# Optimization experiments

Hardware: AMD Instinct MI355X
Metric: run time of the kernel (lower is better)

## Reference

```python
import jax, jax.numpy as jnp
import numpy as np

EMB_DIM = 2048
USER_DIM = 256
NUM_EXPERTS = 64
TOP_K = 8
N_TOKENS = 16384


def setup_inputs() -> dict:
    key = jax.random.key(0)
    k_h, k_u, k_w = jax.random.split(key, 3)
    h = jax.random.normal(k_h, (N_TOKENS, EMB_DIM), dtype=jnp.float32)
    u = jax.random.normal(k_u, (N_TOKENS, USER_DIM), dtype=jnp.float32)
    # nn.Linear weight is [out, in]; we store transposed [in, out] for x @ W
    W = jax.random.normal(k_w, (EMB_DIM + USER_DIM, NUM_EXPERTS), dtype=jnp.float32) * (1.0 / np.sqrt(EMB_DIM + USER_DIM))
    b = jnp.zeros((NUM_EXPERTS,), dtype=jnp.float32)
    return {"h": h, "u": u, "W": W, "b": b}


def reference(h, u, W, b):
    # gate logits: [N, E]
    g = jnp.concatenate([h, u], axis=-1) @ W + b
    w = jax.nn.softmax(g, axis=-1)
    # top-k mask + renormalize (top_k < num_experts)
    _, top_idx = jax.lax.top_k(w, TOP_K)                       # [N, k]
    mask = jax.nn.one_hot(top_idx, NUM_EXPERTS, dtype=w.dtype).sum(axis=-2)  # [N, E]
    w = w * mask
    w = w / (w.sum(axis=-1, keepdims=True) + 1e-9)
    return w
```

## Files before the change

### kernel.cpp

```cpp
#include <hip/hip_runtime.h>

#define EMB 2048
#define UDIM 256
#define KTOT 2304
#define NE 64
#define TOPK 8
#define SSH 6144
#define STEPB 12288
#define KSPL 12
#define SPS 6
#define SLICEB (SPS * STEPB)
#define NB 64
#define NTOK 16384
#define PART_OFF (1 << 20)

typedef __attribute__((ext_vector_type(8))) short short8;
typedef __attribute__((ext_vector_type(4))) float f32x4;
typedef __attribute__((ext_vector_type(4))) unsigned int u32x4;

__device__ __forceinline__ unsigned short bf16h(float x) {
  unsigned uu = __builtin_bit_cast(unsigned, x);
  return (unsigned short)((uu + 0x7FFFu + ((uu >> 16) & 1u)) >> 16);
}
__device__ __forceinline__ float bf2f(unsigned short s) {
  return __builtin_bit_cast(float, ((unsigned)s) << 16);
}

__device__ __forceinline__ unsigned cvtpk(float a, float b) {
  unsigned r;
  asm("v_cvt_pk_bf16_f32 %0, %1, %2" : "=v"(r) : "v"(a), "v"(b));
  return r;
}

__global__ __launch_bounds__(256)
void prep_w(const float* __restrict__ W, unsigned short* __restrict__ wb) {
  const int flat = blockIdx.x * 256 + threadIdx.x;
  const int k = flat >> 6;
  const int n = flat & 63;
  const float w = W[flat];
  const unsigned short h0 = bf16h(w);
  const float r1 = w - bf2f(h0);
  const unsigned short h1 = bf16h(r1);
  const float r2 = r1 - bf2f(h1);
  const unsigned short h2 = bf16h(r2);

  const int s = k >> 5;
  const int kk = k & 31;
  const int lane = (kk >> 3) * 16 + (n & 15);
  const int j = kk & 7;
  const int nt = n >> 4;
  const size_t base = (size_t)s * SSH + ((size_t)nt * 64 + lane) * 8 + j;
  wb[base] = h0;
  wb[base + 2048] = h1;
  wb[base + 4096] = h2;
}

__global__ __launch_bounds__(512, 4)
void gate_split(const float* __restrict__ h, const float* __restrict__ u,
                const unsigned short* __restrict__ wb,
                float* __restrict__ partial) {
  __shared__ __align__(1024) char lds[SLICEB];

  const int tid = threadIdx.x;
  const int lane = tid & 63;
  const int wid = __builtin_amdgcn_readfirstlane(tid >> 6);
  const int kq = blockIdx.x >> 6;
  const int bb = blockIdx.x & 63;
  const int mm = lane & 15;
  const int q8 = (lane >> 4) * 8;

  const char* src = (const char*)wb + (size_t)kq * SLICEB + (size_t)lane * 16;
  for (int j = wid; j < SPS * 12; j += 8)
    __builtin_amdgcn_global_load_lds(
        (const __attribute__((address_space(1))) unsigned int*)(src + (size_t)j * 1024),
        (__attribute__((address_space(3))) unsigned int*)(lds + (size_t)j * 1024),
        16, 0, 0);
  __syncthreads();

  const char* lb = lds + (size_t)lane * 16;
  const int ks0 = kq * SPS;

#pragma unroll 1
  for (int tt = 0; tt < 2; ++tt) {
    const int tile = (bb * 8 + wid) * 2 + tt;
    const int token = tile * 16 + mm;
    const float* hrow = h + (size_t)token * EMB + q8;
    const float* urow = u + (size_t)token * UDIM + q8;

    f32x4 A[2 * SPS];
#pragma unroll
    for (int s = 0; s < SPS; ++s) {
      const int as = ks0 + s;
      const float* bs = (as < 64) ? (hrow + as * 32) : (urow + (as - 64) * 32);
      A[2 * s] = *(const f32x4*)bs;
      A[2 * s + 1] = *(const f32x4*)(bs + 4);
    }
    __builtin_amdgcn_sched_barrier(0);

    f32x4 acc[4];
#pragma unroll
    for (int nt = 0; nt < 4; ++nt) acc[nt] = 0.f;

#pragma unroll
    for (int s = 0; s < SPS; ++s) {
      short8 Bv[12];
#pragma unroll
      for (int q = 0; q < 12; ++q)
        Bv[q] = *(const short8*)(lb + (size_t)s * STEPB + q * 1024);

      const f32x4 c0 = A[2 * s], c1 = A[2 * s + 1];
      const float xs[8] = {c0[0], c0[1], c0[2], c0[3],
                           c1[0], c1[1], c1[2], c1[3]};
      u32x4 W0, W1, W2;
#pragma unroll
      for (int k2 = 0; k2 < 4; ++k2) {
        const float a = xs[2 * k2], bbv = xs[2 * k2 + 1];
        const unsigned p0 = cvtpk(a, bbv);
        const float a1 = a - __builtin_bit_cast(float, p0 << 16);
        const float b1 = bbv - __builtin_bit_cast(float, p0 & 0xFFFF0000u);
        const unsigned p1 = cvtpk(a1, b1);
        const float a2 = a1 - __builtin_bit_cast(float, p1 << 16);
        const float b2 = b1 - __builtin_bit_cast(float, p1 & 0xFFFF0000u);
        const unsigned p2 = cvtpk(a2, b2);
        W0[k2] = p0; W1[k2] = p1; W2[k2] = p2;
      }
      const short8 A0 = __builtin_bit_cast(short8, W0);
      const short8 A1 = __builtin_bit_cast(short8, W1);
      const short8 A2 = __builtin_bit_cast(short8, W2);

#pragma unroll
      for (int nt = 0; nt < 4; ++nt) {
        acc[nt] = __builtin_amdgcn_mfma_f32_16x16x32_bf16(A0, Bv[0 + nt], acc[nt], 0, 0, 0);
        acc[nt] = __builtin_amdgcn_mfma_f32_16x16x32_bf16(A0, Bv[4 + nt], acc[nt], 0, 0, 0);
        acc[nt] = __builtin_amdgcn_mfma_f32_16x16x32_bf16(A1, Bv[0 + nt], acc[nt], 0, 0, 0);
        acc[nt] = __builtin_amdgcn_mfma_f32_16x16x32_bf16(A1, Bv[4 + nt], acc[nt], 0, 0, 0);
        acc[nt] = __builtin_amdgcn_mfma_f32_16x16x32_bf16(A0, Bv[8 + nt], acc[nt], 0, 0, 0);
        acc[nt] = __builtin_amdgcn_mfma_f32_16x16x32_bf16(A2, Bv[0 + nt], acc[nt], 0, 0, 0);
      }
    }

    const int rowb = (lane >> 4) * 4;
#pragma unroll
    for (int nt = 0; nt < 4; ++nt)
#pragma unroll
      for (int r = 0; r < 4; ++r)
        partial[((size_t)kq * NTOK + tile * 16 + rowb + r) * NE + nt * 16 + mm] =
            acc[nt][r];
  }
}

__global__ __launch_bounds__(256)
void finalize(const float* __restrict__ partial, const float* __restrict__ b,
              float* __restrict__ out) {
  const int tid = threadIdx.x;
  const int lane = tid & 63;
  const int wv = tid >> 6;
  const int t = blockIdx.x * 4 + wv;
  const float bias = b[lane];

  float g = bias;
#pragma unroll
  for (int s = 0; s < KSPL; ++s)
    g += partial[((size_t)s * NTOK + t) * NE + lane];

  float m = g;
#pragma unroll
  for (int off = 32; off > 0; off >>= 1)
    m = fmaxf(m, __shfl_xor(m, off));
  float pexp = __expf(g - m);
  float sum = pexp;
#pragma unroll
  for (int off = 32; off > 0; off >>= 1)
    sum += __shfl_xor(sum, off);
  const float pn = pexp / sum;

  float vv = pn;
  float topsum = 0.f;
  int sel = 0;
  for (int r = 0; r < TOPK; ++r) {
    float mv = vv;
    int mi = lane;
#pragma unroll
    for (int off = 32; off > 0; off >>= 1) {
      const float ov = __shfl_xor(mv, off);
      const int oi = __shfl_xor(mi, off);
      if (ov > mv || (ov == mv && oi < mi)) { mv = ov; mi = oi; }
    }
    topsum += mv;
    if (lane == mi) { sel = 1; vv = -1.f; }
  }

  out[(size_t)t * NE + lane] = sel ? pn / (topsum + 1e-9f) : 0.f;
}

extern "C" void kernel_launch(void* const* d_in, const int* in_sizes, int n_in,
                              void* d_out, int out_size, void* d_ws, size_t ws_size,
                              hipStream_t stream) {
  const float* h = (const float*)d_in[0];
  const float* u = (const float*)d_in[1];
  const float* W = (const float*)d_in[2];
  const float* b = (const float*)d_in[3];
  float* out = (float*)d_out;

  unsigned short* wb = (unsigned short*)d_ws;
  float* partial = (float*)((char*)d_ws + PART_OFF);

  hipLaunchKernelGGL(prep_w, dim3(KTOT * NE / 256), dim3(256), 0, stream, W, wb);
  hipLaunchKernelGGL(gate_split, dim3(KSPL * NB), dim3(512), 0, stream,
                     h, u, wb, partial);
  hipLaunchKernelGGL(finalize, dim3(NTOK / 4), dim3(256), 0, stream,
                     partial, b, out);
}
```

Baseline: 260.2 us.

## Use 8 K-splits of 9 steps and process two token tiles concurrently per wave

Reduces the K split from 12 slices of 6 steps to 8 slices of 9 steps. This cuts the number of partial-sum rows written and later re-read by finalize, and enlarges the LDS weight slice per block. Each wave now loads both of its token tiles up front and interleaves their MFMA chains, reusing each LDS weight fragment read for two tiles and gaining ILP. The tail slice handles the last h step plus the u columns explicitly. The cost is more registers and LDS per block, so the launch bound drops to 1 block per CU-level hint, which lowers occupancy and latency hiding.

```diff
diff --git a/kernel.cpp b/kernel.cpp
--- a/kernel.cpp
+++ b/kernel.cpp
@@ -7,8 +7,8 @@
 #define TOPK 8
 #define SSH 6144
 #define STEPB 12288
-#define KSPL 12
-#define SPS 6
+#define KSPL 8
+#define SPS 9
 #define SLICEB (SPS * STEPB)
 #define NB 64
 #define NTOK 16384
@@ -55,7 +55,39 @@
   wb[base + 4096] = h2;
 }
 
-__global__ __launch_bounds__(512, 4)
+__device__ __forceinline__ void step_math(const f32x4& c0, const f32x4& c1,
+                                          const short8* Bv, f32x4* acc) {
+  const float xs[8] = {c0[0], c0[1], c0[2], c0[3],
+                       c1[0], c1[1], c1[2], c1[3]};
+  u32x4 W0, W1, W2;
+#pragma unroll
+  for (int k2 = 0; k2 < 4; ++k2) {
+    const float a = xs[2 * k2], bbv = xs[2 * k2 + 1];
+    const unsigned p0 = cvtpk(a, bbv);
+    const float a1 = a - __builtin_bit_cast(float, p0 << 16);
+    const float b1 = bbv - __builtin_bit_cast(float, p0 & 0xFFFF0000u);
+    const unsigned p1 = cvtpk(a1, b1);
+    const float a2 = a1 - __builtin_bit_cast(float, p1 << 16);
+    const float b2 = b1 - __builtin_bit_cast(float, p1 & 0xFFFF0000u);
+    const unsigned p2 = cvtpk(a2, b2);
+    W0[k2] = p0; W1[k2] = p1; W2[k2] = p2;
+  }
+  const short8 A0 = __builtin_bit_cast(short8, W0);
+  const short8 A1 = __builtin_bit_cast(short8, W1);
+  const short8 A2 = __builtin_bit_cast(short8, W2);
+
+#pragma unroll
+  for (int nt = 0; nt < 4; ++nt) {
+    acc[nt] = __builtin_amdgcn_mfma_f32_16x16x32_bf16(A0, Bv[0 + nt], acc[nt], 0, 0, 0);
+    acc[nt] = __builtin_amdgcn_mfma_f32_16x16x32_bf16(A0, Bv[4 + nt], acc[nt], 0, 0, 0);
+    acc[nt] = __builtin_amdgcn_mfma_f32_16x16x32_bf16(A1, Bv[0 + nt], acc[nt], 0, 0, 0);
+    acc[nt] = __builtin_amdgcn_mfma_f32_16x16x32_bf16(A1, Bv[4 + nt], acc[nt], 0, 0, 0);
+    acc[nt] = __builtin_amdgcn_mfma_f32_16x16x32_bf16(A0, Bv[8 + nt], acc[nt], 0, 0, 0);
+    acc[nt] = __builtin_amdgcn_mfma_f32_16x16x32_bf16(A2, Bv[0 + nt], acc[nt], 0, 0, 0);
+  }
+}
+
+__global__ __launch_bounds__(512, 1)
 void gate_split(const float* __restrict__ h, const float* __restrict__ u,
                 const unsigned short* __restrict__ wb,
                 float* __restrict__ partial) {
@@ -77,76 +109,60 @@
         16, 0, 0);
   __syncthreads();
 
+  const bool tail = (kq == KSPL - 1);
   const char* lb = lds + (size_t)lane * 16;
   const int ks0 = kq * SPS;
-
-#pragma unroll 1
-  for (int tt = 0; tt < 2; ++tt) {
-    const int tile = (bb * 8 + wid) * 2 + tt;
-    const int token = tile * 16 + mm;
-    const float* hrow = h + (size_t)token * EMB + q8;
-    const float* urow = u + (size_t)token * UDIM + q8;
-
-    f32x4 A[2 * SPS];
-#pragma unroll
-    for (int s = 0; s < SPS; ++s) {
-      const int as = ks0 + s;
-      const float* bs = (as < 64) ? (hrow + as * 32) : (urow + (as - 64) * 32);
-      A[2 * s] = *(const f32x4*)bs;
-      A[2 * s + 1] = *(const f32x4*)(bs + 4);
+  const int tb = (bb * 8 + wid) * 2;
+
+  const int tok0 = (tb + 0) * 16 + mm;
+  const int tok1 = (tb + 1) * 16 + mm;
+  const float* hr0 = h + (size_t)tok0 * EMB + q8;
+  const float* ur0 = u + (size_t)tok0 * UDIM + q8;
+  const float* hr1 = h + (size_t)tok1 * EMB + q8;
+  const float* ur1 = u + (size_t)tok1 * UDIM + q8;
+
+  f32x4 acc0[4], acc1[4];
+#pragma unroll
+  for (int nt = 0; nt < 4; ++nt) { acc0[nt] = 0.f; acc1[nt] = 0.f; }
+
+  f32x4 Aa[2 * SPS], Ab[2 * SPS];
+#pragma unroll
+  for (int s = 0; s < SPS; ++s) {
+    const float* p0;
+    const float* p1;
+    if (!tail) {
+      p0 = hr0 + (ks0 + s) * 32;
+      p1 = hr1 + (ks0 + s) * 32;
+    } else {
+      p0 = (s == 0) ? (hr0 + 2016) : (ur0 + (s - 1) * 32);
+      p1 = (s == 0) ? (hr1 + 2016) : (ur1 + (s - 1) * 32);
     }
-    __builtin_amdgcn_sched_barrier(0);
-
-    f32x4 acc[4];
-#pragma unroll
-    for (int nt = 0; nt < 4; ++nt) acc[nt] = 0.f;
-
-#pragma unroll
-    for (int s = 0; s < SPS; ++s) {
-      short8 Bv[12];
-#pragma unroll
-      for (int q = 0; q < 12; ++q)
-        Bv[q] = *(const short8*)(lb + (size_t)s * STEPB + q * 1024);
-
-      const f32x4 c0 = A[2 * s], c1 = A[2 * s + 1];
-      const float xs[8] = {c0[0], c0[1], c0[2], c0[3],
-                           c1[0], c1[1], c1[2], c1[3]};
-      u32x4 W0, W1, W2;
-#pragma unroll
-      for (int k2 = 0; k2 < 4; ++k2) {
-        const float a = xs[2 * k2], bbv = xs[2 * k2 + 1];
-        const unsigned p0 = cvtpk(a, bbv);
-        const float a1 = a - __builtin_bit_cast(float, p0 << 16);
-        const float b1 = bbv - __builtin_bit_cast(float, p0 & 0xFFFF0000u);
-        const unsigned p1 = cvtpk(a1, b1);
-        const float a2 = a1 - __builtin_bit_cast(float, p1 << 16);
-        const float b2 = b1 - __builtin_bit_cast(float, p1 & 0xFFFF0000u);
-        const unsigned p2 = cvtpk(a2, b2);
-        W0[k2] = p0; W1[k2] = p1; W2[k2] = p2;
-      }
-      const short8 A0 = __builtin_bit_cast(short8, W0);
-      const short8 A1 = __builtin_bit_cast(short8, W1);
-      const short8 A2 = __builtin_bit_cast(short8, W2);
-
-#pragma unroll
-      for (int nt = 0; nt < 4; ++nt) {
-        acc[nt] = __builtin_amdgcn_mfma_f32_16x16x32_bf16(A0, Bv[0 + nt], acc[nt], 0, 0, 0);
-        acc[nt] = __builtin_amdgcn_mfma_f32_16x16x32_bf16(A0, Bv[4 + nt], acc[nt], 0, 0, 0);
-        acc[nt] = __builtin_amdgcn_mfma_f32_16x16x32_bf16(A1, Bv[0 + nt], acc[nt], 0, 0, 0);
-        acc[nt] = __builtin_amdgcn_mfma_f32_16x16x32_bf16(A1, Bv[4 + nt], acc[nt], 0, 0, 0);
-        acc[nt] = __builtin_amdgcn_mfma_f32_16x16x32_bf16(A0, Bv[8 + nt], acc[nt], 0, 0, 0);
-        acc[nt] = __builtin_amdgcn_mfma_f32_16x16x32_bf16(A2, Bv[0 + nt], acc[nt], 0, 0, 0);
-      }
+    Aa[2 * s] = *(const f32x4*)p0;
+    Aa[2 * s + 1] = *(const f32x4*)(p0 + 4);
+    Ab[2 * s] = *(const f32x4*)p1;
+    Ab[2 * s + 1] = *(const f32x4*)(p1 + 4);
+  }
+
+#pragma unroll
+  for (int s = 0; s < SPS; ++s) {
+    short8 Bv[12];
+#pragma unroll
+    for (int q = 0; q < 12; ++q)
+      Bv[q] = *(const short8*)(lb + (size_t)s * STEPB + q * 1024);
+    step_math(Aa[2 * s], Aa[2 * s + 1], Bv, acc0);
+    step_math(Ab[2 * s], Ab[2 * s + 1], Bv, acc1);
+  }
+
+  const int rowb = (lane >> 4) * 4;
+#pragma unroll
+  for (int nt = 0; nt < 4; ++nt)
+#pragma unroll
+    for (int r = 0; r < 4; ++r) {
+      partial[((size_t)kq * NTOK + (tb + 0) * 16 + rowb + r) * NE + nt * 16 + mm] =
+          acc0[nt][r];
+      partial[((size_t)kq * NTOK + (tb + 1) * 16 + rowb + r) * NE + nt * 16 + mm] =
+          acc1[nt][r];
     }
-
-    const int rowb = (lane >> 4) * 4;
-#pragma unroll
-    for (int nt = 0; nt < 4; ++nt)
-#pragma unroll
-      for (int r = 0; r < 4; ++r)
-        partial[((size_t)kq * NTOK + tile * 16 + rowb + r) * NE + nt * 16 + mm] =
-            acc[nt][r];
-  }
 }
 
 __global__ __launch_bounds__(256)
```

New measurement: 270.0 us. 3.8% more time.
